# Performance work log

Hardware: AMD Instinct MI355X
Metric: run time of the kernel (lower is better)

The kernel has to match this reference:

```python
import jax, jax.numpy as jnp
import numpy as np

HEADS = 16
DIM_HEAD = 128
DIM = HEADS * DIM_HEAD          # hidden_size = 2048
SEGMENT_LEN = 496
NUM_LONGTERM = 16
NUM_PERSIST = 16
C = SEGMENT_LEN + NUM_LONGTERM  # total_segment_len = 512 (window width)
EPS = 1e-6
THETA = 10000.0
NEG = -jnp.finfo(jnp.float32).max


def _rope(t, cos, sin):
    # t: [b, h, n, d]; cos/sin: [n, d]; interleaved (rotate-half on adjacent pairs)
    t2 = t.reshape(t.shape[:-1] + (DIM_HEAD // 2, 2))
    rot = jnp.stack((-t2[..., 1], t2[..., 0]), axis=-1).reshape(t.shape)
    return t * cos + rot * sin


def _attn_bias():
    # queries: [m_len longterm-mem tokens | segment tokens]
    # keys:    [p_len persistent | m_len longterm-mem | segment tokens]
    q_len = C
    k_len = C + NUM_PERSIST
    pq = NUM_LONGTERM
    pk = NUM_PERSIST + NUM_LONGTERM
    bias = jnp.full((q_len, k_len), NEG, dtype=jnp.float32)
    bias = bias.at[:, :pk].set(0.0)  # everyone attends to the prefix
    sq = q_len - pq
    causal = jnp.tril(jnp.ones((sq, sq), dtype=bool))
    bias = bias.at[pq:, pk:].set(jnp.where(causal, 0.0, NEG))
    return bias


def setup_inputs() -> dict:
    key = jax.random.key(0)
    k1, k2, k3, k4 = jax.random.split(key, 4)
    b, n = 2, 4096  # n must be a multiple of C=512
    return {
        "x": jax.random.normal(k1, (b, n, DIM), dtype=jnp.float32),
        "norm_w": jnp.ones((DIM,), dtype=jnp.float32),
        "w_qkv": jax.random.normal(k2, (3 * DIM, DIM), dtype=jnp.float32) * 0.02,
        "w_out": jax.random.normal(k3, (DIM, DIM), dtype=jnp.float32) * 0.02,
        "pm": jax.random.normal(k4, (2, HEADS, NUM_PERSIST, DIM_HEAD), dtype=jnp.float32) * 0.02,
    }


def reference(x, norm_w, w_qkv, w_out, pm):
    b, n, d = x.shape
    # RMSNorm
    xn = x * jax.lax.rsqrt(jnp.mean(x * x, axis=-1, keepdims=True) + EPS) * norm_w
    # qkv projection (Linear, no bias)
    qkv = xn @ w_qkv.T
    q, k, v = jnp.split(qkv, 3, axis=-1)

    def to_heads(t):  # [b, n, h*d] -> [b, h, n, d]
        return t.reshape(b, n, HEADS, DIM_HEAD).transpose(0, 2, 1, 3)

    q, k, v = to_heads(q), to_heads(k), to_heads(v)

    # RoPE over full sequence positions 0..n-1 (before windowing)
    inv_freq = 1.0 / (THETA ** (jnp.arange(0, DIM_HEAD, 2, dtype=jnp.float32) / DIM_HEAD))
    freqs = jnp.arange(n, dtype=jnp.float32)[:, None] * inv_freq  # [n, d/2]
    freqs = jnp.repeat(freqs, 2, axis=-1)                          # [n, d]
    cos, sin = jnp.cos(freqs), jnp.sin(freqs)
    q = _rope(q, cos, sin)
    k = _rope(k, cos, sin)

    # split into windows of width C: [b, h, n, d] -> [(b*w), h, C, d]
    w = n // C

    def to_windows(t):
        return t.reshape(b, HEADS, w, C, DIM_HEAD).transpose(0, 2, 1, 3, 4).reshape(b * w, HEADS, C, DIM_HEAD)

    q, k, v = to_windows(q), to_windows(k), to_windows(v)

    # prepend persistent memory tokens to k, v
    pmk = jnp.broadcast_to(pm[0], (b * w, HEADS, NUM_PERSIST, DIM_HEAD))
    pmv = jnp.broadcast_to(pm[1], (b * w, HEADS, NUM_PERSIST, DIM_HEAD))
    k = jnp.concatenate((pmk, k), axis=-2)  # [(b*w), h, C+P, d]
    v = jnp.concatenate((pmv, v), axis=-2)

    bias = _attn_bias()  # [C, C+P]
    scale = DIM_HEAD ** -0.5
    sim = jnp.einsum('whqd,whkd->whqk', q, k) * scale + bias
    attn = jax.nn.softmax(sim, axis=-1)
    out = jnp.einsum('whqk,whkd->whqd', attn, v)

    # '(b w) h c d -> b (w c) (h d)'
    out = out.reshape(b, w, HEADS, C, DIM_HEAD).transpose(0, 1, 3, 2, 4).reshape(b, n, HEADS * DIM_HEAD)
    return out @ w_out.T
```

## Files before the change

### kernel.cpp

```cpp
#include <hip/hip_runtime.h>
#include <hip/hip_bf16.h>

typedef __attribute__((ext_vector_type(8))) short short8v;
typedef __attribute__((ext_vector_type(4))) float f32x4;
typedef __attribute__((ext_vector_type(4))) unsigned short us4;

#define DEV static __device__ __forceinline__

DEV unsigned short f2bf(float f) {
  unsigned u = __builtin_bit_cast(unsigned, f);
  u += 0x7FFFu + ((u >> 16) & 1u);
  return (unsigned short)(u >> 16);
}
DEV float bf2f(unsigned short s) {
  unsigned u = ((unsigned)s) << 16;
  return __builtin_bit_cast(float, u);
}
DEV void gload16(const void* g, void* l) {
  __builtin_amdgcn_global_load_lds((const __attribute__((address_space(1))) void*)g,
                                   (__attribute__((address_space(3))) void*)l, 16, 0, 0);
}

__global__ __launch_bounds__(256) void k_cvt(const float* __restrict__ s,
                                             unsigned short* __restrict__ d, long n4) {
  long i = (long)blockIdx.x * 256 + threadIdx.x;
  if (i >= n4) return;
  f32x4 v = *((const f32x4*)s + i);
  us4 o;
  o[0] = f2bf(v[0]); o[1] = f2bf(v[1]); o[2] = f2bf(v[2]); o[3] = f2bf(v[3]);
  *((us4*)d + i) = o;
}

__global__ __launch_bounds__(256) void k_pmprep(const float* __restrict__ pm,
                                                unsigned short* __restrict__ pmk,
                                                unsigned short* __restrict__ vt,
                                                unsigned short* __restrict__ zbuf) {
  int idx = blockIdx.x * 256 + threadIdx.x;
  if (idx < 8) zbuf[idx] = 0;
  if (idx >= 16 * 16 * 128) return;
  int d = idx & 127, p = (idx >> 7) & 15, h = idx >> 11;
  float kvl = pm[((0 * 16 + h) * 16 + p) * 128 + d];
  float vvl = pm[((1 * 16 + h) * 16 + p) * 128 + d];
  pmk[(h * 16 + p) * 128 + d] = f2bf(kvl);
  unsigned short vb = f2bf(vvl);
  for (int w = 0; w < 16; ++w) {
    long base = ((long)(w * 16 + h) * 128 + d) * 544;
    vt[base + p] = vb;
    vt[base + 528 + p] = 0;
  }
}

__global__ __launch_bounds__(256) void k_ropetab(float* __restrict__ ct, float* __restrict__ st) {
  int idx = blockIdx.x * 256 + threadIdx.x;
  int pos = idx >> 6, i = idx & 63;
  float invf = __powf(10000.f, -(float)i * (1.f / 64.f));
  float a = (float)pos * invf;
  ct[idx] = cosf(a);
  st[idx] = sinf(a);
}

__global__ __launch_bounds__(256) void k_rms(const float* __restrict__ x,
                                             const float* __restrict__ w,
                                             unsigned short* __restrict__ xb) {
  int row = blockIdx.x, tid = threadIdx.x;
  const f32x4* xr = (const f32x4*)(x + (long)row * 2048);
  f32x4 v0 = xr[tid * 2], v1 = xr[tid * 2 + 1];
  float ss = v0[0]*v0[0] + v0[1]*v0[1] + v0[2]*v0[2] + v0[3]*v0[3]
           + v1[0]*v1[0] + v1[1]*v1[1] + v1[2]*v1[2] + v1[3]*v1[3];
  ss += __shfl_xor(ss, 1);  ss += __shfl_xor(ss, 2);  ss += __shfl_xor(ss, 4);
  ss += __shfl_xor(ss, 8);  ss += __shfl_xor(ss, 16); ss += __shfl_xor(ss, 32);
  __shared__ float red[4];
  if ((tid & 63) == 0) red[tid >> 6] = ss;
  __syncthreads();
  float tot = red[0] + red[1] + red[2] + red[3];
  float rs = rsqrtf(tot * (1.f / 2048.f) + 1e-6f);
  float xv[8] = {v0[0], v0[1], v0[2], v0[3], v1[0], v1[1], v1[2], v1[3]};
  short8v pack;
#pragma unroll
  for (int j = 0; j < 8; ++j) pack[j] = (short)f2bf(xv[j] * rs * w[tid * 8 + j]);
  *((short8v*)(xb + (long)row * 2048) + tid) = pack;
}


#define VMCNT4 asm volatile("s_waitcnt vmcnt(4)" ::: "memory")
#define VMCNT0 asm volatile("s_waitcnt vmcnt(0)" ::: "memory")
#define SCHEDB __builtin_amdgcn_sched_barrier(0)
#define NOSTG ((void)0)

template <int OUTF32>
__global__ __launch_bounds__(512, 2) void k_gemm8(const unsigned short* __restrict__ A,
                                                  const unsigned short* __restrict__ B,
                                                  unsigned short* __restrict__ Cb,
                                                  float* __restrict__ Cf,
                                                  int M, int N, int K) {
  __shared__ __align__(16) unsigned short lds[4 * 256 * 64];
  const int tid = threadIdx.x;
  const int lane = tid & 63;
  const int ql = lane & 15, g = lane >> 4;
  const int wid = tid >> 6;
  const int wm = wid >> 2, wn = wid & 3;

  const int nbx = N >> 8;
  const int nwg = gridDim.x;
  int bid = blockIdx.x;
  int swz = (bid & 7) * (nwg >> 3) + (bid >> 3);
  int by = swz / nbx, bx = swz - by * nbx;
  const long rowA0 = (long)by << 8;
  const long rowB0 = (long)bx << 8;

  const int idx0 = tid, idx1 = 512 + tid;
  const int dr0 = idx0 >> 3, sc0 = (idx0 & 7) ^ (dr0 & 7);
  const int dr1 = idx1 >> 3, sc1 = (idx1 & 7) ^ (dr1 & 7);
  const long halfA = 128L * K;
  const unsigned short* pA0 = A + (rowA0 + dr0) * (long)K + sc0 * 8;
  const unsigned short* pA1 = A + (rowA0 + dr1) * (long)K + sc1 * 8;
  const unsigned short* pB0 = B + (rowB0 + dr0) * (long)K + sc0 * 8;
  const unsigned short* pB1 = B + (rowB0 + dr1) * (long)K + sc1 * 8;

  const int rsw0 = (g ^ (ql & 7)) * 8;
  const int rsw1 = ((4 + g) ^ (ql & 7)) * 8;

  short8v fa[4], fb[2][4];
  f32x4 acc[8][4] = {};

#define STAGE_A(b, h, kk) do { \
  gload16(pA0 + (long)(h) * halfA + (kk), lds + (b) * 32768 + (h) * 8192 + (idx0 << 3)); \
  gload16(pA1 + (long)(h) * halfA + (kk), lds + (b) * 32768 + (h) * 8192 + (idx1 << 3)); } while (0)
#define STAGE_B(b, h, kk) do { \
  gload16(pB0 + (long)(h) * halfA + (kk), lds + (b) * 32768 + 16384 + (h) * 8192 + (idx0 << 3)); \
  gload16(pB1 + (long)(h) * halfA + (kk), lds + (b) * 32768 + 16384 + (h) * 8192 + (idx1 << 3)); } while (0)

#define PHASE(buf, mh, ks, LOADB, STG, VMC) do { \
  { const unsigned short* p_ = lds + (buf) * 32768 + (((wm << 7) + (mh) * 64 + ql) << 6) + ((ks) ? rsw1 : rsw0); \
    _Pragma("unroll") for (int mi_ = 0; mi_ < 4; ++mi_) fa[mi_] = *(const short8v*)(p_ + (mi_ << 10)); } \
  if (LOADB) { const unsigned short* p_ = lds + (buf) * 32768 + 16384 + (((wn << 6) + ql) << 6) + ((ks) ? rsw1 : rsw0); \
    _Pragma("unroll") for (int n_ = 0; n_ < 4; ++n_) fb[ks][n_] = *(const short8v*)(p_ + (n_ << 10)); } \
  STG; \
  SCHEDB; __builtin_amdgcn_s_barrier(); SCHEDB; \
  __builtin_amdgcn_s_setprio(1); \
  _Pragma("unroll") for (int mi_ = 0; mi_ < 4; ++mi_) \
    _Pragma("unroll") for (int n_ = 0; n_ < 4; ++n_) \
      acc[(mh) * 4 + mi_][n_] = __builtin_amdgcn_mfma_f32_16x16x32_bf16(fa[mi_], fb[ks][n_], acc[(mh) * 4 + mi_][n_], 0, 0, 0); \
  __builtin_amdgcn_s_setprio(0); \
  VMC; \
  SCHEDB; __builtin_amdgcn_s_barrier(); SCHEDB; \
} while (0)

  const int NT = K >> 6;
  const int NITER = NT >> 1;

  STAGE_A(0, 0, 0); STAGE_A(0, 1, 0);
  STAGE_B(0, 0, 0); STAGE_B(0, 1, 0);
  STAGE_B(1, 0, 64); STAGE_B(1, 1, 64);
  VMCNT4;
  SCHEDB; __builtin_amdgcn_s_barrier(); SCHEDB;

  for (int i = 0; i < NITER - 1; ++i) {
    const int k1 = (2 * i + 1) << 6;
    const int k2 = (2 * i + 2) << 6;
    const int k3 = (2 * i + 3) << 6;
    PHASE(0, 0, 0, 1, STAGE_A(1, 0, k1), NOSTG);
    PHASE(0, 0, 1, 1, STAGE_A(1, 1, k1), NOSTG);
    PHASE(0, 1, 0, 0, STAGE_B(0, 0, k2), NOSTG);
    PHASE(0, 1, 1, 0, STAGE_B(0, 1, k2), VMCNT4);
    PHASE(1, 0, 0, 1, STAGE_A(0, 0, k2), NOSTG);
    PHASE(1, 0, 1, 1, STAGE_A(0, 1, k2), NOSTG);
    PHASE(1, 1, 0, 0, STAGE_B(1, 0, k3), NOSTG);
    PHASE(1, 1, 1, 0, STAGE_B(1, 1, k3), VMCNT4);
  }
  {
    const int k1 = (NT - 1) << 6;
    PHASE(0, 0, 0, 1, STAGE_A(1, 0, k1), NOSTG);
    PHASE(0, 0, 1, 1, STAGE_A(1, 1, k1), NOSTG);
    PHASE(0, 1, 0, 0, NOSTG, NOSTG);
    PHASE(0, 1, 1, 0, NOSTG, VMCNT0);
    PHASE(1, 0, 0, 1, NOSTG, NOSTG);
    PHASE(1, 0, 1, 1, NOSTG, NOSTG);
    PHASE(1, 1, 0, 0, NOSTG, NOSTG);
    PHASE(1, 1, 1, 0, NOSTG, NOSTG);
  }

#pragma unroll
  for (int am = 0; am < 8; ++am)
#pragma unroll
    for (int n = 0; n < 4; ++n)
#pragma unroll
      for (int r = 0; r < 4; ++r) {
        long row = rowA0 + (wm << 7) + am * 16 + (g << 2) + r;
        long col = rowB0 + (wn << 6) + n * 16 + ql;
        if (OUTF32) Cf[row * N + col] = acc[am][n][r];
        else        Cb[row * N + col] = f2bf(acc[am][n][r]);
      }
#undef STAGE_A
#undef STAGE_B
#undef PHASE
}

__global__ __launch_bounds__(256) void k_rope(unsigned short* __restrict__ qkv,
                                              const float* __restrict__ ct,
                                              const float* __restrict__ st) {
  long idx = (long)blockIdx.x * 256 + threadIdx.x;
  if (idx >= 8388608L) return;
  int t = (int)(idx >> 10);
  int h = (int)((idx >> 6) & 15);
  int i = (int)(idx & 63);
  int pos = t & 4095;
  float c = ct[pos * 64 + i], s = st[pos * 64 + i];
  long qoff = (long)t * 6144 + h * 128 + 2 * i;
  unsigned q01 = *(const unsigned*)(qkv + qoff);
  float a = bf2f((unsigned short)(q01 & 0xffff)), b = bf2f((unsigned short)(q01 >> 16));
  const float SC = 0.08838834764831845f;
  float ra = (a * c - b * s) * SC, rb = (b * c + a * s) * SC;
  *(unsigned*)(qkv + qoff) = (unsigned)f2bf(ra) | ((unsigned)f2bf(rb) << 16);
  long koff = qoff + 2048;
  unsigned k01 = *(const unsigned*)(qkv + koff);
  a = bf2f((unsigned short)(k01 & 0xffff)); b = bf2f((unsigned short)(k01 >> 16));
  ra = a * c - b * s; rb = b * c + a * s;
  *(unsigned*)(qkv + koff) = (unsigned)f2bf(ra) | ((unsigned)f2bf(rb) << 16);
}

__global__ __launch_bounds__(256) void k_vtb(const unsigned short* __restrict__ qkv,
                                             unsigned short* __restrict__ vt) {
  __shared__ unsigned short lt[64 * 136];
  int tile = blockIdx.x, h = blockIdx.y;
  int tid = threadIdx.x;
  int t0 = tile * 64;
  {
    int row = tid >> 2, seg = tid & 3;
    const unsigned short* src = qkv + (long)(t0 + row) * 6144 + 4096 + h * 128 + seg * 32;
#pragma unroll
    for (int j = 0; j < 4; ++j)
      *(short8v*)(lt + row * 136 + seg * 32 + j * 8) = *(const short8v*)(src + j * 8);
  }
  __syncthreads();
  int d = tid >> 1, half = tid & 1;
  int wh = t0 >> 9;
  long dst = ((long)(wh * 16 + h) * 128 + d) * 544 + (t0 & 511) + 16 + half * 32;
  unsigned short tmp[32];
#pragma unroll
  for (int kk = 0; kk < 32; ++kk) tmp[kk] = lt[(half * 32 + kk) * 136 + d];
#pragma unroll
  for (int j = 0; j < 4; ++j) {
    short8v v;
#pragma unroll
    for (int e = 0; e < 8; ++e) v[e] = (short)tmp[j * 8 + e];
    *(short8v*)(vt + dst + j * 8) = v;
  }
}

__global__ __launch_bounds__(256) void k_attn(const unsigned short* __restrict__ qkv,
                                              const unsigned short* __restrict__ vt,
                                              const unsigned short* __restrict__ pmk,
                                              const unsigned short* __restrict__ zbuf,
                                              unsigned short* __restrict__ attno) {
  __shared__ __align__(16) unsigned short Ks[32 * 128];
  __shared__ __align__(16) unsigned short Vs[128 * 32];
  const int qb = blockIdx.x, wh = blockIdx.y, h = blockIdx.z;
  const int tid = threadIdx.x;
  const int wave = tid >> 6, lane = tid & 63;
  const int ql = lane & 15, g = lane >> 4;
  const int tokbase = (wh >> 3) * 4096 + (wh & 7) * 512;
  const int qi = qb * 64 + wave * 16 + ql;
  const long qrow = (long)(tokbase + qi) * 6144;
  short8v qf[4];
#pragma unroll
  for (int ks = 0; ks < 4; ++ks)
    qf[ks] = *(const short8v*)(qkv + qrow + h * 128 + ks * 32 + g * 8);
  float mrun = -3.0e38f, lrun = 0.f;
  f32x4 o[8] = {};
  const int nkt = min(17, (qb * 64 + 64 + 16 + 31) >> 5);
  const long vbase = ((long)(wh * 16 + h) * 128) * 544;
  for (int kt = 0; kt < nkt; ++kt) {
#pragma unroll
    for (int i = 0; i < 2; ++i) {
      int c = i * 256 + tid;
      int kl = c >> 4, dc = c & 15;
      int dcs = dc ^ (kl & 7);
      int ki = kt * 32 + kl;
      const unsigned short* src;
      if (ki < 16)       src = pmk + (h * 16 + ki) * 128 + dcs * 8;
      else if (ki < 528) src = qkv + (long)(tokbase + ki - 16) * 6144 + 2048 + h * 128 + dcs * 8;
      else               src = zbuf;
      gload16(src, Ks + (size_t)(i * 256 + wave * 64) * 8);
    }
#pragma unroll
    for (int i = 0; i < 2; ++i) {
      int c = i * 256 + tid;
      int d = c >> 2, kc = c & 3;
      int kcs = kc ^ (d & 3);
      gload16(vt + vbase + (long)d * 544 + kt * 32 + kcs * 8, Vs + (size_t)(i * 256 + wave * 64) * 8);
    }
    __syncthreads();
    f32x4 st[2] = {};
#pragma unroll
    for (int kf = 0; kf < 2; ++kf) {
      int row = kf * 16 + ql;
#pragma unroll
      for (int ks = 0; ks < 4; ++ks) {
        int dchunk = (ks * 4 + g) ^ (row & 7);
        short8v kv = *(const short8v*)(Ks + row * 128 + dchunk * 8);
        st[kf] = __builtin_amdgcn_mfma_f32_16x16x32_bf16(kv, qf[ks], st[kf], 0, 0, 0);
      }
    }
    float tmax = -3.0e38f;
#pragma unroll
    for (int kf = 0; kf < 2; ++kf)
#pragma unroll
      for (int r = 0; r < 4; ++r) {
        int ki = kt * 32 + kf * 16 + g * 4 + r;
        bool ok = (ki < 32) || (qi >= 16 && ki <= qi + 16);
        float s = ok ? st[kf][r] : -3.0e38f;
        st[kf][r] = s;
        tmax = fmaxf(tmax, s);
      }
    tmax = fmaxf(tmax, __shfl_xor(tmax, 16));
    tmax = fmaxf(tmax, __shfl_xor(tmax, 32));
    float mnew = fmaxf(mrun, tmax);
    float corr = __expf(mrun - mnew);
    float psum = 0.f;
#pragma unroll
    for (int kf = 0; kf < 2; ++kf)
#pragma unroll
      for (int r = 0; r < 4; ++r) {
        float p = __expf(st[kf][r] - mnew);
        st[kf][r] = p;
        psum += p;
      }
    psum += __shfl_xor(psum, 16);
    psum += __shfl_xor(psum, 32);
    lrun = lrun * corr + psum;
    mrun = mnew;
#pragma unroll
    for (int db = 0; db < 8; ++db) {
      o[db][0] *= corr; o[db][1] *= corr; o[db][2] *= corr; o[db][3] *= corr;
    }
    short8v pb;
#pragma unroll
    for (int j = 0; j < 8; ++j) {
      int srcl = ((((g & 1) * 2 + (j >> 2))) << 4) | ql;
      float v0 = __shfl(st[0][j & 3], srcl);
      float v1 = __shfl(st[1][j & 3], srcl);
      pb[j] = (short)f2bf((g >> 1) ? v1 : v0);
    }
#pragma unroll
    for (int db = 0; db < 8; ++db) {
      int d = db * 16 + ql;
      int kc = g ^ (d & 3);
      short8v vf = *(const short8v*)(Vs + d * 32 + kc * 8);
      o[db] = __builtin_amdgcn_mfma_f32_16x16x32_bf16(vf, pb, o[db], 0, 0, 0);
    }
    __syncthreads();
  }
  float inv = 1.0f / lrun;
  long obase = (long)(tokbase + qi) * 2048 + h * 128;
#pragma unroll
  for (int db = 0; db < 8; ++db)
#pragma unroll
    for (int r = 0; r < 4; ++r)
      attno[obase + db * 16 + g * 4 + r] = f2bf(o[db][r] * inv);
}

extern "C" void kernel_launch(void* const* d_in, const int* in_sizes, int n_in,
                              void* d_out, int out_size, void* d_ws, size_t ws_size,
                              hipStream_t stream) {
  const float* x      = (const float*)d_in[0];
  const float* norm_w = (const float*)d_in[1];
  const float* w_qkv  = (const float*)d_in[2];
  const float* w_out  = (const float*)d_in[3];
  const float* pm     = (const float*)d_in[4];
  float* out = (float*)d_out;

  char* ws = (char*)d_ws;
  size_t off = 0;
  auto alloc = [&](size_t bytes) -> void* {
    void* p = ws + off;
    off += (bytes + 255) & ~(size_t)255;
    return p;
  };
  unsigned short* xb    = (unsigned short*)alloc(8192ull * 2048 * 2);
  unsigned short* wqkvb = (unsigned short*)alloc(6144ull * 2048 * 2);
  unsigned short* woutb = (unsigned short*)alloc(2048ull * 2048 * 2);
  unsigned short* qkv   = (unsigned short*)alloc(8192ull * 6144 * 2);
  unsigned short* vt    = (unsigned short*)alloc(256ull * 128 * 544 * 2);
  unsigned short* attno = (unsigned short*)alloc(8192ull * 2048 * 2);
  unsigned short* pmk   = (unsigned short*)alloc(16 * 16 * 128 * 2);
  float* ct             = (float*)alloc(4096 * 64 * 4);
  float* stt            = (float*)alloc(4096 * 64 * 4);
  unsigned short* zbuf  = (unsigned short*)alloc(256);

  hipLaunchKernelGGL(k_cvt, dim3(12288), dim3(256), 0, stream, w_qkv, wqkvb, 3145728L);
  hipLaunchKernelGGL(k_cvt, dim3(4096), dim3(256), 0, stream, w_out, woutb, 1048576L);
  hipLaunchKernelGGL(k_pmprep, dim3(128), dim3(256), 0, stream, pm, pmk, vt, zbuf);
  hipLaunchKernelGGL(k_ropetab, dim3(1024), dim3(256), 0, stream, ct, stt);
  hipLaunchKernelGGL(k_rms, dim3(8192), dim3(256), 0, stream, x, norm_w, xb);
  hipLaunchKernelGGL((k_gemm8<0>), dim3(24 * 32), dim3(512), 0, stream,
                     xb, wqkvb, qkv, (float*)nullptr, 8192, 6144, 2048);
  hipLaunchKernelGGL(k_rope, dim3(32768), dim3(256), 0, stream, qkv, ct, stt);
  hipLaunchKernelGGL(k_vtb, dim3(128, 16), dim3(256), 0, stream, qkv, vt);
  hipLaunchKernelGGL(k_attn, dim3(8, 16, 16), dim3(256), 0, stream, qkv, vt, pmk, zbuf, attno);
  hipLaunchKernelGGL((k_gemm8<1>), dim3(8 * 32), dim3(512), 0, stream,
                     attno, woutb, (unsigned short*)nullptr, out, 8192, 2048, 2048);
}
```

Before: 448.1 us.

## Double-buffer attention K/V tiles, widen blocks to 128 queries, skip masked tiles

Restructures the attention kernel to use 512-thread blocks covering 128 queries each, with double-buffered LDS for K and V tiles. The next tile is prefetched while the current one is computed, so only one barrier is needed per iteration. Each wave now skips key tiles that lie wholly beyond its causal range. It also applies a lazy max-rescale, so the output correction runs only when the running max grows by more than a threshold. The V-transpose row stride is padded from 544 to 576 so the extra prefetch reads past the window stay in bounds and zero-filled, at the cost of more LDS per block and fewer blocks in the grid.

```diff
diff --git a/kernel.cpp b/kernel.cpp
--- a/kernel.cpp
+++ b/kernel.cpp
@@ -44,9 +44,11 @@
   pmk[(h * 16 + p) * 128 + d] = f2bf(kvl);
   unsigned short vb = f2bf(vvl);
   for (int w = 0; w < 16; ++w) {
-    long base = ((long)(w * 16 + h) * 128 + d) * 544;
+    long base = ((long)(w * 16 + h) * 128 + d) * 576;
     vt[base + p] = vb;
     vt[base + 528 + p] = 0;
+    vt[base + 544 + p] = 0;
+    vt[base + 560 + p] = 0;
   }
 }
 
@@ -235,7 +237,7 @@
   __syncthreads();
   int d = tid >> 1, half = tid & 1;
   int wh = t0 >> 9;
-  long dst = ((long)(wh * 16 + h) * 128 + d) * 544 + (t0 & 511) + 16 + half * 32;
+  long dst = ((long)(wh * 16 + h) * 128 + d) * 576 + (t0 & 511) + 16 + half * 32;
   unsigned short tmp[32];
 #pragma unroll
   for (int kk = 0; kk < 32; ++kk) tmp[kk] = lt[(half * 32 + kk) * 136 + d];
@@ -248,109 +250,114 @@
   }
 }
 
-__global__ __launch_bounds__(256) void k_attn(const unsigned short* __restrict__ qkv,
+__global__ __launch_bounds__(512) void k_attn(const unsigned short* __restrict__ qkv,
                                               const unsigned short* __restrict__ vt,
                                               const unsigned short* __restrict__ pmk,
                                               const unsigned short* __restrict__ zbuf,
                                               unsigned short* __restrict__ attno) {
-  __shared__ __align__(16) unsigned short Ks[32 * 128];
-  __shared__ __align__(16) unsigned short Vs[128 * 32];
+  __shared__ __align__(16) unsigned short Ks[2][32 * 128];
+  __shared__ __align__(16) unsigned short Vs[2][128 * 32];
   const int qb = blockIdx.x, wh = blockIdx.y, h = blockIdx.z;
   const int tid = threadIdx.x;
   const int wave = tid >> 6, lane = tid & 63;
   const int ql = lane & 15, g = lane >> 4;
   const int tokbase = (wh >> 3) * 4096 + (wh & 7) * 512;
-  const int qi = qb * 64 + wave * 16 + ql;
+  const int qi = qb * 128 + wave * 16 + ql;
+  const int wqmax = qb * 128 + wave * 16 + 15;
   const long qrow = (long)(tokbase + qi) * 6144;
   short8v qf[4];
 #pragma unroll
   for (int ks = 0; ks < 4; ++ks)
     qf[ks] = *(const short8v*)(qkv + qrow + h * 128 + ks * 32 + g * 8);
+  const int nkt = min(17, (qb * 128 + 144 + 31) >> 5);
+  const long vbase = (long)(wh * 16 + h) * 128 * 576;
+
   float mrun = -3.0e38f, lrun = 0.f;
   f32x4 o[8] = {};
-  const int nkt = min(17, (qb * 64 + 64 + 16 + 31) >> 5);
-  const long vbase = ((long)(wh * 16 + h) * 128) * 544;
+
+#define STAGEKV(kt, b) do { \
+    { int kl_ = tid >> 4, dc_ = tid & 15, dcs_ = dc_ ^ (kl_ & 7); \
+      int ki_ = (kt) * 32 + kl_; \
+      const unsigned short* src_; \
+      if (ki_ < 16)       src_ = pmk + (h * 16 + ki_) * 128 + dcs_ * 8; \
+      else if (ki_ < 528) src_ = qkv + (long)(tokbase + ki_ - 16) * 6144 + 2048 + h * 128 + dcs_ * 8; \
+      else                src_ = zbuf; \
+      gload16(src_, &Ks[b][0] + (size_t)tid * 8); } \
+    { int d_ = tid >> 2, kc_ = tid & 3, kcs_ = kc_ ^ (d_ & 3); \
+      gload16(vt + vbase + (long)d_ * 576 + (kt) * 32 + kcs_ * 8, &Vs[b][0] + (size_t)tid * 8); } \
+  } while (0)
+
+  STAGEKV(0, 0);
+  __syncthreads();
   for (int kt = 0; kt < nkt; ++kt) {
-#pragma unroll
-    for (int i = 0; i < 2; ++i) {
-      int c = i * 256 + tid;
-      int kl = c >> 4, dc = c & 15;
-      int dcs = dc ^ (kl & 7);
-      int ki = kt * 32 + kl;
-      const unsigned short* src;
-      if (ki < 16)       src = pmk + (h * 16 + ki) * 128 + dcs * 8;
-      else if (ki < 528) src = qkv + (long)(tokbase + ki - 16) * 6144 + 2048 + h * 128 + dcs * 8;
-      else               src = zbuf;
-      gload16(src, Ks + (size_t)(i * 256 + wave * 64) * 8);
-    }
-#pragma unroll
-    for (int i = 0; i < 2; ++i) {
-      int c = i * 256 + tid;
-      int d = c >> 2, kc = c & 3;
-      int kcs = kc ^ (d & 3);
-      gload16(vt + vbase + (long)d * 544 + kt * 32 + kcs * 8, Vs + (size_t)(i * 256 + wave * 64) * 8);
+    const int cur = kt & 1;
+    if (kt + 1 < nkt) STAGEKV(kt + 1, cur ^ 1);
+    if (kt * 32 <= wqmax + 16) {
+      f32x4 stv[2] = {};
+#pragma unroll
+      for (int kf = 0; kf < 2; ++kf) {
+        int row = kf * 16 + ql;
+#pragma unroll
+        for (int ks = 0; ks < 4; ++ks) {
+          int chunk = (ks * 4 + g) ^ (row & 7);
+          short8v kv = *(const short8v*)(&Ks[cur][0] + row * 128 + chunk * 8);
+          stv[kf] = __builtin_amdgcn_mfma_f32_16x16x32_bf16(kv, qf[ks], stv[kf], 0, 0, 0);
+        }
+      }
+      float tmax = -3.0e38f;
+#pragma unroll
+      for (int kf = 0; kf < 2; ++kf)
+#pragma unroll
+        for (int r = 0; r < 4; ++r) {
+          int ki = kt * 32 + kf * 16 + g * 4 + r;
+          bool ok = (ki < 32) || (qi >= 16 && ki <= qi + 16);
+          float s = ok ? stv[kf][r] : -3.0e38f;
+          stv[kf][r] = s;
+          tmax = fmaxf(tmax, s);
+        }
+      tmax = fmaxf(tmax, __shfl_xor(tmax, 16));
+      tmax = fmaxf(tmax, __shfl_xor(tmax, 32));
+      if (!__all(tmax <= mrun + 8.f)) {
+        float mnew = fmaxf(mrun, tmax);
+        float corr = __expf(mrun - mnew);
+        lrun *= corr;
+#pragma unroll
+        for (int db = 0; db < 8; ++db) {
+          o[db][0] *= corr; o[db][1] *= corr; o[db][2] *= corr; o[db][3] *= corr;
+        }
+        mrun = mnew;
+      }
+      float psum = 0.f;
+#pragma unroll
+      for (int kf = 0; kf < 2; ++kf)
+#pragma unroll
+        for (int r = 0; r < 4; ++r) {
+          float p = __expf(stv[kf][r] - mrun);
+          stv[kf][r] = p;
+          psum += p;
+        }
+      psum += __shfl_xor(psum, 16);
+      psum += __shfl_xor(psum, 32);
+      lrun += psum;
+      short8v pb;
+#pragma unroll
+      for (int j = 0; j < 8; ++j) {
+        int srcl = (((g & 1) * 2 + (j >> 2)) << 4) | ql;
+        float v0 = __shfl(stv[0][j & 3], srcl);
+        float v1 = __shfl(stv[1][j & 3], srcl);
+        pb[j] = (short)f2bf((g >> 1) ? v1 : v0);
+      }
+#pragma unroll
+      for (int db = 0; db < 8; ++db) {
+        int d = db * 16 + ql;
+        int kc = g ^ (d & 3);
+        short8v vf = *(const short8v*)(&Vs[cur][0] + d * 32 + kc * 8);
+        o[db] = __builtin_amdgcn_mfma_f32_16x16x32_bf16(vf, pb, o[db], 0, 0, 0);
+      }
     }
     __syncthreads();
-    f32x4 st[2] = {};
-#pragma unroll
-    for (int kf = 0; kf < 2; ++kf) {
-      int row = kf * 16 + ql;
-#pragma unroll
-      for (int ks = 0; ks < 4; ++ks) {
-        int dchunk = (ks * 4 + g) ^ (row & 7);
-        short8v kv = *(const short8v*)(Ks + row * 128 + dchunk * 8);
-        st[kf] = __builtin_amdgcn_mfma_f32_16x16x32_bf16(kv, qf[ks], st[kf], 0, 0, 0);
-      }
-    }
-    float tmax = -3.0e38f;
-#pragma unroll
-    for (int kf = 0; kf < 2; ++kf)
-#pragma unroll
-      for (int r = 0; r < 4; ++r) {
-        int ki = kt * 32 + kf * 16 + g * 4 + r;
-        bool ok = (ki < 32) || (qi >= 16 && ki <= qi + 16);
-        float s = ok ? st[kf][r] : -3.0e38f;
-        st[kf][r] = s;
-        tmax = fmaxf(tmax, s);
-      }
-    tmax = fmaxf(tmax, __shfl_xor(tmax, 16));
-    tmax = fmaxf(tmax, __shfl_xor(tmax, 32));
-    float mnew = fmaxf(mrun, tmax);
-    float corr = __expf(mrun - mnew);
-    float psum = 0.f;
-#pragma unroll
-    for (int kf = 0; kf < 2; ++kf)
-#pragma unroll
-      for (int r = 0; r < 4; ++r) {
-        float p = __expf(st[kf][r] - mnew);
-        st[kf][r] = p;
-        psum += p;
-      }
-    psum += __shfl_xor(psum, 16);
-    psum += __shfl_xor(psum, 32);
-    lrun = lrun * corr + psum;
-    mrun = mnew;
-#pragma unroll
-    for (int db = 0; db < 8; ++db) {
-      o[db][0] *= corr; o[db][1] *= corr; o[db][2] *= corr; o[db][3] *= corr;
-    }
-    short8v pb;
-#pragma unroll
-    for (int j = 0; j < 8; ++j) {
-      int srcl = ((((g & 1) * 2 + (j >> 2))) << 4) | ql;
-      float v0 = __shfl(st[0][j & 3], srcl);
-      float v1 = __shfl(st[1][j & 3], srcl);
-      pb[j] = (short)f2bf((g >> 1) ? v1 : v0);
-    }
-#pragma unroll
-    for (int db = 0; db < 8; ++db) {
-      int d = db * 16 + ql;
-      int kc = g ^ (d & 3);
-      short8v vf = *(const short8v*)(Vs + d * 32 + kc * 8);
-      o[db] = __builtin_amdgcn_mfma_f32_16x16x32_bf16(vf, pb, o[db], 0, 0, 0);
-    }
-    __syncthreads();
-  }
+  }
+#undef STAGEKV
   float inv = 1.0f / lrun;
   long obase = (long)(tokbase + qi) * 2048 + h * 128;
 #pragma unroll
@@ -381,7 +388,7 @@
   unsigned short* wqkvb = (unsigned short*)alloc(6144ull * 2048 * 2);
   unsigned short* woutb = (unsigned short*)alloc(2048ull * 2048 * 2);
   unsigned short* qkv   = (unsigned short*)alloc(8192ull * 6144 * 2);
-  unsigned short* vt    = (unsigned short*)alloc(256ull * 128 * 544 * 2);
+  unsigned short* vt    = (unsigned short*)alloc(256ull * 128 * 576 * 2);
   unsigned short* attno = (unsigned short*)alloc(8192ull * 2048 * 2);
   unsigned short* pmk   = (unsigned short*)alloc(16 * 16 * 128 * 2);
   float* ct             = (float*)alloc(4096 * 64 * 4);
@@ -397,7 +404,7 @@
                      xb, wqkvb, qkv, (float*)nullptr, 8192, 6144, 2048);
   hipLaunchKernelGGL(k_rope, dim3(32768), dim3(256), 0, stream, qkv, ct, stt);
   hipLaunchKernelGGL(k_vtb, dim3(128, 16), dim3(256), 0, stream, qkv, vt);
-  hipLaunchKernelGGL(k_attn, dim3(8, 16, 16), dim3(256), 0, stream, qkv, vt, pmk, zbuf, attno);
+  hipLaunchKernelGGL(k_attn, dim3(4, 16, 16), dim3(512), 0, stream, qkv, vt, pmk, zbuf, attno);
   hipLaunchKernelGGL((k_gemm8<1>), dim3(8 * 32), dim3(512), 0, stream,
                      attno, woutb, (unsigned short*)nullptr, out, 8192, 2048, 2048);
 }
```

New measurement: 432.6 us. -3.5%, faster.
